# Optimization experiments

Hardware: AMD Instinct MI355X
Metric: run time of the kernel (lower is better)

Reference implementation:

```python
import jax, jax.numpy as jnp
import numpy as np

N_NODES = 100000
N_EDGES = 1600000
F_IN = 128
HIDDEN = 128
N_CLASSES = 2
N_GRAPHS = 512


def setup_inputs() -> dict:
    key = jax.random.key(0)
    ks = jax.random.split(key, 10)
    node_features = jax.random.normal(ks[0], (N_NODES, F_IN), dtype=jnp.float32)
    edge_index = jax.random.randint(ks[1], (2, N_EDGES), 0, N_NODES, dtype=jnp.int64)
    batch = jnp.sort(jax.random.randint(ks[2], (N_NODES,), 0, N_GRAPHS, dtype=jnp.int64))
    s1 = 1.0 / np.sqrt(F_IN)
    s2 = 1.0 / np.sqrt(HIDDEN)
    W1 = jax.random.uniform(ks[3], (F_IN, HIDDEN), jnp.float32, -s1, s1)
    b1 = jnp.zeros((HIDDEN,), jnp.float32)
    W2 = jax.random.uniform(ks[4], (HIDDEN, HIDDEN), jnp.float32, -s2, s2)
    b2 = jnp.zeros((HIDDEN,), jnp.float32)
    Wlin = jax.random.uniform(ks[5], (HIDDEN, N_CLASSES), jnp.float32, -s2, s2)
    blin = jax.random.uniform(ks[6], (N_CLASSES,), jnp.float32, -s2, s2)
    return {"node_features": node_features, "edge_index": edge_index, "batch": batch,
            "W1": W1, "b1": b1, "W2": W2, "b2": b2, "Wlin": Wlin, "blin": blin}


def _gcn_conv(x, src, dst, norm, W, b, n_nodes):
    # transform-then-propagate (PyG GCNConv default)
    h = x @ W                                   # [N, H]
    msg = h[src] * norm[:, None]                # gather + edge scale
    out = jax.ops.segment_sum(msg, dst, num_segments=n_nodes)  # scatter-add
    return out + b


def reference(node_features, edge_index, batch, W1, b1, W2, b2, Wlin, blin):
    n = node_features.shape[0]
    loop = jnp.arange(n, dtype=edge_index.dtype)
    src = jnp.concatenate([edge_index[0], loop])  # add self-loops
    dst = jnp.concatenate([edge_index[1], loop])
    # symmetric degree normalization: deg counts incoming edges incl. self-loop
    deg = jax.ops.segment_sum(jnp.ones_like(src, dtype=node_features.dtype), dst, num_segments=n)
    dis = jnp.where(deg > 0, jax.lax.rsqrt(jnp.maximum(deg, 1.0)), 0.0)
    norm = dis[src] * dis[dst]

    x = jax.nn.relu(_gcn_conv(node_features, src, dst, norm, W1, b1, n))
    x = jax.nn.relu(_gcn_conv(x, src, dst, norm, W2, b2, n))

    # global mean pool over graphs
    ones = jnp.ones((n,), dtype=x.dtype)
    counts = jax.ops.segment_sum(ones, batch, num_segments=N_GRAPHS)
    sums = jax.ops.segment_sum(x, batch, num_segments=N_GRAPHS)
    pooled = sums / jnp.maximum(counts, 1.0)[:, None]

    # dropout is identity in eval mode
    return pooled @ Wlin + blin
```

## Files before the change

### kernel.cpp

```cpp
#include <hip/hip_runtime.h>
#include <hip/hip_bf16.h>
#include <hip/hip_fp16.h>

constexpr int NN = 100000;
constexpr int NE = 1600000;
constexpr int NG = 512;
constexpr int F  = 128;

constexpr int NB   = 392;
constexpr int RCAP = 4608;
constexpr int CAP  = 32;
constexpr int NCH  = 8;
constexpr int BINB = 512;
constexpr int GEMB = (NN + 127) / 128;

typedef _Float16 f16;
typedef f16 f16x2 __attribute__((ext_vector_type(2)));
typedef f16 f16x4 __attribute__((ext_vector_type(4)));
typedef f16 f16x8 __attribute__((ext_vector_type(8)));
typedef float f32x4 __attribute__((ext_vector_type(4)));
typedef unsigned int u32;
typedef u32 u32x4a __attribute__((ext_vector_type(4), aligned(4)));

template<bool IN_HALF>
__device__ __forceinline__ void gemm_body(int bid, int tid,
                                          const void* __restrict__ Xv,
                                          const f16* __restrict__ WT,
                                          const float* __restrict__ dis,
                                          f16* __restrict__ H, int M) {
    const int wid = tid >> 6;
    const int lane = tid & 63;
    const int row0 = bid * 128;
    const int wrow = wid * 32;
    const int lr = lane & 15;
    const int lk = (lane >> 4) * 8;
    f32x4 acc[2][8] = {};
    #pragma unroll
    for (int ks = 0; ks < 4; ks++) {
        f16x8 a[2], b[8];
        #pragma unroll
        for (int mf = 0; mf < 2; mf++) {
            int row = row0 + wrow + mf * 16 + lr;
            row = row < M ? row : M - 1;
            if (IN_HALF) {
                a[mf] = *(const f16x8*)((const f16*)Xv + (size_t)row * 128 + ks * 32 + lk);
            } else {
                const float* Xf = (const float*)Xv + (size_t)row * 128 + ks * 32 + lk;
                float4 v0 = *(const float4*)Xf;
                float4 v1 = *(const float4*)(Xf + 4);
                a[mf] = f16x8{(f16)v0.x, (f16)v0.y, (f16)v0.z, (f16)v0.w,
                              (f16)v1.x, (f16)v1.y, (f16)v1.z, (f16)v1.w};
            }
        }
        #pragma unroll
        for (int nf = 0; nf < 8; nf++)
            b[nf] = *(const f16x8*)(WT + (size_t)(nf * 16 + lr) * 128 + ks * 32 + lk);
        #pragma unroll
        for (int mf = 0; mf < 2; mf++)
            #pragma unroll
            for (int nf = 0; nf < 8; nf++)
                acc[mf][nf] = __builtin_amdgcn_mfma_f32_16x16x32_f16(a[mf], b[nf], acc[mf][nf], 0, 0, 0);
    }
    const int crow = (lane >> 4) * 4;
    #pragma unroll
    for (int mf = 0; mf < 2; mf++) {
        #pragma unroll
        for (int reg = 0; reg < 4; reg++) {
            int row = row0 + wrow + mf * 16 + crow + reg;
            if (row < M) {
                float sc = dis[row];
                #pragma unroll
                for (int nf = 0; nf < 8; nf++)
                    H[(size_t)row * 128 + nf * 16 + lr] = (f16)(acc[mf][nf][reg] * sc);
            }
        }
    }
}

__global__ __launch_bounds__(256) void k1_bin_prepw(const int* __restrict__ ei,
                                                    int* __restrict__ gcur,
                                                    u32* __restrict__ binned,
                                                    const float* __restrict__ W1,
                                                    const float* __restrict__ W2,
                                                    f16* __restrict__ WT1,
                                                    f16* __restrict__ WT2) {
    __shared__ u32 stage[NB][CAP];
    __shared__ int scnt[NB];
    if (blockIdx.x >= BINB) {
        int idx = (blockIdx.x - BINB) * 256 + threadIdx.x;
        int n = idx >> 7, k = idx & 127;
        WT1[idx] = (f16)W1[k * 128 + n];
        WT2[idx] = (f16)W2[k * 128 + n];
        return;
    }
    for (int b = threadIdx.x; b < NB; b += 256) scnt[b] = 0;
    __syncthreads();
    const int per = NE / BINB;
    const int e0 = blockIdx.x * per;
    for (int r = 0; r < per; r += 256) {
        int k = r + threadIdx.x;
        if (k < per) {
            int e = e0 + k;
            int s = __builtin_nontemporal_load(&ei[e]);
            int d = __builtin_nontemporal_load(&ei[NE + e]);
            int b = d >> 8;
            u32 v = ((u32)(d & 255) << 24) | (u32)s;
            int p = atomicAdd(&scnt[b], 1);
            if (p < CAP) stage[b][p] = v;
        }
        __syncthreads();
        for (int b2 = threadIdx.x; b2 < NB; b2 += 256) {
            int n = scnt[b2];
            if (n >= 16) {
                int f = n & ~15;
                int base = b2 * RCAP + atomicAdd(&gcur[b2], f);
                const u32x4a* st4 = (const u32x4a*)&stage[b2][0];
                u32x4a* out4 = (u32x4a*)&binned[base];
                for (int j = 0; j < (f >> 2); j++) out4[j] = st4[j];
                for (int j = 0; j < n - f; j++) stage[b2][j] = stage[b2][f + j];
                scnt[b2] = n - f;
            }
        }
        __syncthreads();
    }
    for (int b2 = threadIdx.x; b2 < NB; b2 += 256) {
        int n = scnt[b2];
        if (n > 0) {
            int base = b2 * RCAP + atomicAdd(&gcur[b2], n);
            for (int j = 0; j < n; j++) binned[base + j] = stage[b2][j];
        }
    }
}

__global__ void scan_buckets(const int* __restrict__ gcur, int* __restrict__ bucketBase,
                             int* __restrict__ offs) {
    __shared__ int tmp[512];
    int t = threadIdx.x;
    int c = (t < NB) ? gcur[t] : 0;
    tmp[t] = c;
    __syncthreads();
    for (int d = 1; d < 512; d <<= 1) {
        int x = (t >= d) ? tmp[t - d] : 0;
        __syncthreads();
        tmp[t] += x;
        __syncthreads();
    }
    if (t < NB) bucketBase[t] = tmp[t] - c;
    if (t == 0) offs[NN] = NE;
}

__global__ __launch_bounds__(256) void k3_csr_gemm1(const u32* __restrict__ binned,
                                                    const int* __restrict__ gcur,
                                                    const int* __restrict__ bucketBase,
                                                    int* __restrict__ offs,
                                                    float* __restrict__ dis,
                                                    int* __restrict__ csr_src,
                                                    const float* __restrict__ X,
                                                    const f16* __restrict__ WT1,
                                                    const float* __restrict__ degdis,
                                                    f16* __restrict__ H) {
    __shared__ u32 ed[RCAP];
    __shared__ u32 lcsr[RCAP];
    __shared__ int hist[256];
    __shared__ int loff[256];
    __shared__ int lcur[256];
    if (blockIdx.x >= NB) {
        gemm_body<false>(blockIdx.x - NB, threadIdx.x, X, WT1, degdis, H, NN);
        return;
    }
    const int b = blockIdx.x;
    int cnt = gcur[b];
    if (cnt > RCAP) cnt = RCAP;
    const int gbase = bucketBase[b];
    const int t = threadIdx.x;
    hist[t] = 0;
    __syncthreads();
    for (int j = t; j < cnt; j += 256) {
        u32 v = __builtin_nontemporal_load(&binned[(size_t)b * RCAP + j]);
        ed[j] = v;
        atomicAdd(&hist[v >> 24], 1);
    }
    __syncthreads();
    int h = hist[t];
    loff[t] = h;
    __syncthreads();
    for (int d = 1; d < 256; d <<= 1) {
        int x = (t >= d) ? loff[t - d] : 0;
        __syncthreads();
        loff[t] += x;
        __syncthreads();
    }
    int excl = loff[t] - h;
    lcur[t] = excl;
    int node = (b << 8) + t;
    if (node < NN) {
        offs[node] = gbase + excl;
        dis[node] = rsqrtf((float)(h + 1));
    }
    __syncthreads();
    for (int j = t; j < cnt; j += 256) {
        u32 v = ed[j];
        int p = atomicAdd(&lcur[v >> 24], 1);
        lcsr[p] = v & 0x1FFFFu;
    }
    __syncthreads();
    for (int j = t; j < cnt; j += 256) csr_src[gbase + j] = (int)lcsr[j];
}


__device__ __forceinline__ void gather_rows_scaled(const f16* __restrict__ h, int i,
                                                   const int* __restrict__ offs,
                                                   const int* __restrict__ csr_src,
                                                   const float* __restrict__ dis,
                                                   int q, int r, float acc[8]) {
    if (q == 0) {
        f16x8 v = *(const f16x8*)(h + (size_t)i * F + r * 8);
        float di = dis[i];
        #pragma unroll
        for (int j = 0; j < 8; j++) acc[j] = (float)v[j] * di;
    }
    const int s = offs[i], e = offs[i + 1];
    int t = s + q;
    for (; t + 4 < e; t += 8) {
        int sr0 = csr_src[t];
        int sr1 = csr_src[t + 4];
        float d0 = dis[sr0], d1 = dis[sr1];
        f16x8 v0 = *(const f16x8*)(h + (size_t)sr0 * F + r * 8);
        f16x8 v1 = *(const f16x8*)(h + (size_t)sr1 * F + r * 8);
        #pragma unroll
        for (int j = 0; j < 8; j++)
            acc[j] += (float)v0[j] * d0 + (float)v1[j] * d1;
    }
    if (t < e) {
        int sr = csr_src[t];
        float d0 = dis[sr];
        f16x8 v = *(const f16x8*)(h + (size_t)sr * F + r * 8);
        #pragma unroll
        for (int j = 0; j < 8; j++) acc[j] += (float)v[j] * d0;
    }
    #pragma unroll
    for (int j = 0; j < 8; j++) {
        acc[j] += __shfl_xor(acc[j], 16);
        acc[j] += __shfl_xor(acc[j], 32);
    }
}

__device__ __forceinline__ void gather_rows(const f16* __restrict__ h, int i,
                                            const int* __restrict__ offs,
                                            const int* __restrict__ csr_src,
                                            int q, int r, float acc[8]) {
    if (q == 0) {
        f16x8 v = *(const f16x8*)(h + (size_t)i * F + r * 8);
        #pragma unroll
        for (int j = 0; j < 8; j++) acc[j] = (float)v[j];
    }
    const int s = offs[i], e = offs[i + 1];
    int t = s + q;
    for (; t + 4 < e; t += 8) {
        int sr0 = csr_src[t];
        int sr1 = csr_src[t + 4];
        f16x8 v0 = *(const f16x8*)(h + (size_t)sr0 * F + r * 8);
        f16x8 v1 = *(const f16x8*)(h + (size_t)sr1 * F + r * 8);
        #pragma unroll
        for (int j = 0; j < 8; j++) acc[j] += (float)v0[j] + (float)v1[j];
    }
    if (t < e) {
        int sr = csr_src[t];
        f16x8 v = *(const f16x8*)(h + (size_t)sr * F + r * 8);
        #pragma unroll
        for (int j = 0; j < 8; j++) acc[j] += (float)v[j];
    }
    #pragma unroll
    for (int j = 0; j < 8; j++) {
        acc[j] += __shfl_xor(acc[j], 16);
        acc[j] += __shfl_xor(acc[j], 32);
    }
}

__global__ __launch_bounds__(256) void aggregate_l1(const f16* __restrict__ h,
                                                    const int* __restrict__ offs,
                                                    const int* __restrict__ csr_src,
                                                    const float* __restrict__ dis,
                                                    const float* __restrict__ bias,
                                                    f16* __restrict__ out, int n) {
    int i = blockIdx.x * 4 + (threadIdx.x >> 6);
    if (i >= n) return;
    const int lane = threadIdx.x & 63;
    const int q = lane >> 4;
    const int r = lane & 15;
    float acc[8] = {};
    gather_rows_scaled(h, i, offs, csr_src, dis, q, r, acc);
    if (q == 0) {
        float di = dis[i];
        const float4* b4 = (const float4*)bias;
        float4 bb0 = b4[r * 2], bb1 = b4[r * 2 + 1];
        float bb[8] = {bb0.x, bb0.y, bb0.z, bb0.w, bb1.x, bb1.y, bb1.z, bb1.w};
        f16x8 o;
        #pragma unroll
        for (int j = 0; j < 8; j++) {
            float v = fmaf(acc[j], di, bb[j]);
            o[j] = (f16)(v > 0.f ? v : 0.f);
        }
        *(f16x8*)(out + (size_t)i * F + r * 8) = o;
    }
}

__global__ __launch_bounds__(256) void aggregate_l2(const f16* __restrict__ h,
                                                    const int* __restrict__ offs,
                                                    const int* __restrict__ csr_src,
                                                    const float* __restrict__ dis,
                                                    const float* __restrict__ bias,
                                                    f16* __restrict__ out, int n) {
    int i = blockIdx.x * 4 + (threadIdx.x >> 6);
    if (i >= n) return;
    const int lane = threadIdx.x & 63;
    const int q = lane >> 4;
    const int r = lane & 15;
    float acc[8] = {};
    gather_rows(h, i, offs, csr_src, q, r, acc);
    if (q == 0) {
        float di = dis[i];
        const float4* b4 = (const float4*)bias;
        float4 bb0 = b4[r * 2], bb1 = b4[r * 2 + 1];
        float bb[8] = {bb0.x, bb0.y, bb0.z, bb0.w, bb1.x, bb1.y, bb1.z, bb1.w};
        f16x8 o;
        #pragma unroll
        for (int j = 0; j < 8; j++) {
            float v = fmaf(acc[j], di, bb[j]);
            o[j] = (f16)(v > 0.f ? v : 0.f);
        }
        *(f16x8*)(out + (size_t)i * F + r * 8) = o;
    }
}

__global__ __launch_bounds__(256) void gemm2(const f16* __restrict__ Xh,
                                             const f16* __restrict__ WT,
                                             const float* __restrict__ dis,
                                             f16* __restrict__ H, int M) {
    gemm_body<true>(blockIdx.x, threadIdx.x, Xh, WT, dis, H, M);
}

__global__ __launch_bounds__(256) void pool_partial(const f16* __restrict__ x,
                                                    const int* __restrict__ batch,
                                                    float* __restrict__ partial, int n) {
    int g = blockIdx.x;
    __shared__ int se[2];
    if (threadIdx.x < 2) {
        int target = g + threadIdx.x;
        int lo = 0, hi = n;
        while (lo < hi) {
            int mid = (lo + hi) >> 1;
            if (batch[mid] < target) lo = mid + 1; else hi = mid;
        }
        se[threadIdx.x] = lo;
    }
    __syncthreads();
    int s = se[0], e = se[1];
    int wid = threadIdx.x >> 6, lane = threadIdx.x & 63;
    int slot = blockIdx.y * 4 + wid;
    float a0 = 0.f, a1 = 0.f;
    const f16x2* x2 = (const f16x2*)x;
    for (int i = s + slot; i < e; i += 4 * NCH) {
        f16x2 v = x2[(size_t)i * 64 + lane];
        a0 += (float)v[0];
        a1 += (float)v[1];
    }
    __shared__ float red[4][128];
    red[wid][lane * 2] = a0;
    red[wid][lane * 2 + 1] = a1;
    __syncthreads();
    if (wid == 0) {
        float s0 = red[0][lane * 2] + red[1][lane * 2] + red[2][lane * 2] + red[3][lane * 2];
        float s1 = red[0][lane * 2 + 1] + red[1][lane * 2 + 1] + red[2][lane * 2 + 1] + red[3][lane * 2 + 1];
        float2* pp = (float2*)&partial[((size_t)g * NCH + blockIdx.y) * F];
        pp[lane] = make_float2(s0, s1);
    }
}

__global__ __launch_bounds__(128) void pool_final(const float* __restrict__ partial,
                                                  const int* __restrict__ batch,
                                                  const float* __restrict__ Wlin,
                                                  const float* __restrict__ blin,
                                                  float* __restrict__ out, int n) {
    int g = blockIdx.x;
    int f = threadIdx.x;
    __shared__ int se[2];
    if (threadIdx.x < 2) {
        int target = g + threadIdx.x;
        int lo = 0, hi = n;
        while (lo < hi) {
            int mid = (lo + hi) >> 1;
            if (batch[mid] < target) lo = mid + 1; else hi = mid;
        }
        se[threadIdx.x] = lo;
    }
    __syncthreads();
    int s = se[0], e = se[1];
    float acc = 0.f;
    #pragma unroll
    for (int c = 0; c < NCH; c++) acc += partial[((size_t)g * NCH + c) * F + f];
    float cnt = (float)((e - s) > 0 ? (e - s) : 1);
    float p = acc / cnt;
    float v0 = p * Wlin[f * 2 + 0];
    float v1 = p * Wlin[f * 2 + 1];
    #pragma unroll
    for (int o = 32; o > 0; o >>= 1) {
        v0 += __shfl_xor(v0, o);
        v1 += __shfl_xor(v1, o);
    }
    __shared__ float red[4];
    int wid = threadIdx.x >> 6;
    if ((threadIdx.x & 63) == 0) { red[wid * 2] = v0; red[wid * 2 + 1] = v1; }
    __syncthreads();
    if (threadIdx.x == 0) {
        out[g * 2 + 0] = red[0] + red[2] + blin[0];
        out[g * 2 + 1] = red[1] + red[3] + blin[1];
    }
}

extern "C" void kernel_launch(void* const* d_in, const int* in_sizes, int n_in,
                              void* d_out, int out_size, void* d_ws, size_t ws_size,
                              hipStream_t stream) {
    const float* X     = (const float*)d_in[0];
    const int*   ei    = (const int*)d_in[1];
    const int*   batch = (const int*)d_in[2];
    const float* W1    = (const float*)d_in[3];
    const float* b1    = (const float*)d_in[4];
    const float* W2    = (const float*)d_in[5];
    const float* b2    = (const float*)d_in[6];
    const float* Wlin  = (const float*)d_in[7];
    const float* blin  = (const float*)d_in[8];
    float* out = (float*)d_out;

    char* p = (char*)d_ws;
    auto alloc = [&](size_t bytes) -> char* {
        char* r = p;
        p += (bytes + 255) & ~size_t(255);
        return r;
    };
    int*   gcur       = (int*)alloc((size_t)NB * 4);
    int*   bucketBase = (int*)alloc((size_t)NB * 4);
    int*   offs       = (int*)alloc((size_t)(NN + 1) * 4);
    float* dis        = (float*)alloc((size_t)NN * 4);
    u32*   binned     = (u32*)alloc((size_t)NB * RCAP * 4);
    int*   csr_src    = (int*)alloc((size_t)NE * 4);
    f16*   WT1        = (f16*)alloc((size_t)128 * 128 * 2);
    f16*   WT2        = (f16*)alloc((size_t)128 * 128 * 2);
    f16*   bufA       = (f16*)alloc((size_t)NN * F * 2);
    f16*   bufB       = (f16*)alloc((size_t)NN * F * 2);
    float* partial    = (float*)alloc((size_t)NG * NCH * F * 4);
    float* ones       = (float*)alloc((size_t)NN * 4);

    hipMemsetAsync(gcur, 0, (size_t)NB * 4, stream);
    extern __global__ void fill_ones(float*, int);
    fill_ones<<<(NN + 255) / 256, 256, 0, stream>>>(ones, NN);

    k1_bin_prepw<<<BINB + 64, 256, 0, stream>>>(ei, gcur, binned, W1, W2, WT1, WT2);
    scan_buckets<<<1, 512, 0, stream>>>(gcur, bucketBase, offs);
    k3_csr_gemm1<<<NB + GEMB, 256, 0, stream>>>(binned, gcur, bucketBase, offs, dis,
                                                csr_src, X, WT1, ones, bufA);

    aggregate_l1<<<(NN + 3) / 4, 256, 0, stream>>>(bufA, offs, csr_src, dis, b1, bufB, NN);
    gemm2<<<GEMB, 256, 0, stream>>>(bufB, WT2, dis, bufA, NN);
    aggregate_l2<<<(NN + 3) / 4, 256, 0, stream>>>(bufA, offs, csr_src, dis, b2, bufB, NN);
    pool_partial<<<dim3(NG, NCH), 256, 0, stream>>>(bufB, batch, partial, NN);
    pool_final<<<NG, 128, 0, stream>>>(partial, batch, Wlin, blin, out, NN);
}

__global__ void fill_ones(float* __restrict__ v, int n) {
    int i = blockIdx.x * blockDim.x + threadIdx.x;
    if (i < n) v[i] = 1.0f;
}
```

Measured before the change: 262.7 us.

## Fuse layer-1 aggregation with GEMM2 and layer-2 aggregation with pooling

Layer-1 aggregation now writes each wave's 32 output rows into shared memory, and GEMM2 runs on them in the same kernel. This removes a full N×128 fp16 round-trip and one launch. Layer-2 aggregation accumulates per-graph sums in registers and flushes them with atomics into a single partial buffer, which replaces the separate pool_partial kernel and its second buffer read. The fill_ones kernel is dropped by templating away the scale in GEMM1. The cost is much fewer aggregation waves in flight (each wave walks 32 rows serially instead of one), which may hurt latency hiding for the random gathers, plus float atomic contention and non-deterministic summation order.

```diff
diff --git a/kernel.cpp b/kernel.cpp
--- a/kernel.cpp
+++ b/kernel.cpp
@@ -10,9 +10,9 @@
 constexpr int NB   = 392;
 constexpr int RCAP = 4608;
 constexpr int CAP  = 32;
-constexpr int NCH  = 8;
 constexpr int BINB = 512;
 constexpr int GEMB = (NN + 127) / 128;
+constexpr int F2B  = (NN + 63) / 64;
 
 typedef _Float16 f16;
 typedef f16 f16x2 __attribute__((ext_vector_type(2)));
@@ -21,61 +21,6 @@
 typedef float f32x4 __attribute__((ext_vector_type(4)));
 typedef unsigned int u32;
 typedef u32 u32x4a __attribute__((ext_vector_type(4), aligned(4)));
-
-template<bool IN_HALF>
-__device__ __forceinline__ void gemm_body(int bid, int tid,
-                                          const void* __restrict__ Xv,
-                                          const f16* __restrict__ WT,
-                                          const float* __restrict__ dis,
-                                          f16* __restrict__ H, int M) {
-    const int wid = tid >> 6;
-    const int lane = tid & 63;
-    const int row0 = bid * 128;
-    const int wrow = wid * 32;
-    const int lr = lane & 15;
-    const int lk = (lane >> 4) * 8;
-    f32x4 acc[2][8] = {};
-    #pragma unroll
-    for (int ks = 0; ks < 4; ks++) {
-        f16x8 a[2], b[8];
-        #pragma unroll
-        for (int mf = 0; mf < 2; mf++) {
-            int row = row0 + wrow + mf * 16 + lr;
-            row = row < M ? row : M - 1;
-            if (IN_HALF) {
-                a[mf] = *(const f16x8*)((const f16*)Xv + (size_t)row * 128 + ks * 32 + lk);
-            } else {
-                const float* Xf = (const float*)Xv + (size_t)row * 128 + ks * 32 + lk;
-                float4 v0 = *(const float4*)Xf;
-                float4 v1 = *(const float4*)(Xf + 4);
-                a[mf] = f16x8{(f16)v0.x, (f16)v0.y, (f16)v0.z, (f16)v0.w,
-                              (f16)v1.x, (f16)v1.y, (f16)v1.z, (f16)v1.w};
-            }
-        }
-        #pragma unroll
-        for (int nf = 0; nf < 8; nf++)
-            b[nf] = *(const f16x8*)(WT + (size_t)(nf * 16 + lr) * 128 + ks * 32 + lk);
-        #pragma unroll
-        for (int mf = 0; mf < 2; mf++)
-            #pragma unroll
-            for (int nf = 0; nf < 8; nf++)
-                acc[mf][nf] = __builtin_amdgcn_mfma_f32_16x16x32_f16(a[mf], b[nf], acc[mf][nf], 0, 0, 0);
-    }
-    const int crow = (lane >> 4) * 4;
-    #pragma unroll
-    for (int mf = 0; mf < 2; mf++) {
-        #pragma unroll
-        for (int reg = 0; reg < 4; reg++) {
-            int row = row0 + wrow + mf * 16 + crow + reg;
-            if (row < M) {
-                float sc = dis[row];
-                #pragma unroll
-                for (int nf = 0; nf < 8; nf++)
-                    H[(size_t)row * 128 + nf * 16 + lr] = (f16)(acc[mf][nf][reg] * sc);
-            }
-        }
-    }
-}
 
 __global__ __launch_bounds__(256) void k1_bin_prepw(const int* __restrict__ ei,
                                                     int* __restrict__ gcur,
@@ -149,6 +94,61 @@
     if (t == 0) offs[NN] = NE;
 }
 
+template<bool IN_HALF, bool SCALE>
+__device__ __forceinline__ void gemm_body(int bid, int tid,
+                                          const void* __restrict__ Xv,
+                                          const f16* __restrict__ WT,
+                                          const float* __restrict__ dis,
+                                          f16* __restrict__ H, int M) {
+    const int wid = tid >> 6;
+    const int lane = tid & 63;
+    const int row0 = bid * 128;
+    const int wrow = wid * 32;
+    const int lr = lane & 15;
+    const int lk = (lane >> 4) * 8;
+    f32x4 acc[2][8] = {};
+    #pragma unroll
+    for (int ks = 0; ks < 4; ks++) {
+        f16x8 a[2], b[8];
+        #pragma unroll
+        for (int mf = 0; mf < 2; mf++) {
+            int row = row0 + wrow + mf * 16 + lr;
+            row = row < M ? row : M - 1;
+            if (IN_HALF) {
+                a[mf] = *(const f16x8*)((const f16*)Xv + (size_t)row * 128 + ks * 32 + lk);
+            } else {
+                const float* Xf = (const float*)Xv + (size_t)row * 128 + ks * 32 + lk;
+                float4 v0 = *(const float4*)Xf;
+                float4 v1 = *(const float4*)(Xf + 4);
+                a[mf] = f16x8{(f16)v0.x, (f16)v0.y, (f16)v0.z, (f16)v0.w,
+                              (f16)v1.x, (f16)v1.y, (f16)v1.z, (f16)v1.w};
+            }
+        }
+        #pragma unroll
+        for (int nf = 0; nf < 8; nf++)
+            b[nf] = *(const f16x8*)(WT + (size_t)(nf * 16 + lr) * 128 + ks * 32 + lk);
+        #pragma unroll
+        for (int mf = 0; mf < 2; mf++)
+            #pragma unroll
+            for (int nf = 0; nf < 8; nf++)
+                acc[mf][nf] = __builtin_amdgcn_mfma_f32_16x16x32_f16(a[mf], b[nf], acc[mf][nf], 0, 0, 0);
+    }
+    const int crow = (lane >> 4) * 4;
+    #pragma unroll
+    for (int mf = 0; mf < 2; mf++) {
+        #pragma unroll
+        for (int reg = 0; reg < 4; reg++) {
+            int row = row0 + wrow + mf * 16 + crow + reg;
+            if (row < M) {
+                float sc = SCALE ? dis[row] : 1.0f;
+                #pragma unroll
+                for (int nf = 0; nf < 8; nf++)
+                    H[(size_t)row * 128 + nf * 16 + lr] = (f16)(acc[mf][nf][reg] * sc);
+            }
+        }
+    }
+}
+
 __global__ __launch_bounds__(256) void k3_csr_gemm1(const u32* __restrict__ binned,
                                                     const int* __restrict__ gcur,
                                                     const int* __restrict__ bucketBase,
@@ -157,7 +157,6 @@
                                                     int* __restrict__ csr_src,
                                                     const float* __restrict__ X,
                                                     const f16* __restrict__ WT1,
-                                                    const float* __restrict__ degdis,
                                                     f16* __restrict__ H) {
     __shared__ u32 ed[RCAP];
     __shared__ u32 lcsr[RCAP];
@@ -165,7 +164,7 @@
     __shared__ int loff[256];
     __shared__ int lcur[256];
     if (blockIdx.x >= NB) {
-        gemm_body<false>(blockIdx.x - NB, threadIdx.x, X, WT1, degdis, H, NN);
+        gemm_body<false, false>(blockIdx.x - NB, threadIdx.x, X, WT1, nullptr, H, NN);
         return;
     }
     const int b = blockIdx.x;
@@ -206,7 +205,6 @@
     __syncthreads();
     for (int j = t; j < cnt; j += 256) csr_src[gbase + j] = (int)lcsr[j];
 }
-
 
 __device__ __forceinline__ void gather_rows_scaled(const f16* __restrict__ h, int i,
                                                    const int* __restrict__ offs,
@@ -277,103 +275,116 @@
     }
 }
 
-__global__ __launch_bounds__(256) void aggregate_l1(const f16* __restrict__ h,
-                                                    const int* __restrict__ offs,
-                                                    const int* __restrict__ csr_src,
-                                                    const float* __restrict__ dis,
-                                                    const float* __restrict__ bias,
-                                                    f16* __restrict__ out, int n) {
-    int i = blockIdx.x * 4 + (threadIdx.x >> 6);
-    if (i >= n) return;
+__global__ __launch_bounds__(256) void fused_agg1_gemm2(const f16* __restrict__ h1,
+                                                        const int* __restrict__ offs,
+                                                        const int* __restrict__ csr_src,
+                                                        const float* __restrict__ dis,
+                                                        const float* __restrict__ bias,
+                                                        const f16* __restrict__ WT2,
+                                                        f16* __restrict__ H, int n) {
+    __shared__ f16 sX[4][32 * 136];
+    const int wid = threadIdx.x >> 6;
     const int lane = threadIdx.x & 63;
     const int q = lane >> 4;
     const int r = lane & 15;
-    float acc[8] = {};
-    gather_rows_scaled(h, i, offs, csr_src, dis, q, r, acc);
-    if (q == 0) {
-        float di = dis[i];
-        const float4* b4 = (const float4*)bias;
-        float4 bb0 = b4[r * 2], bb1 = b4[r * 2 + 1];
-        float bb[8] = {bb0.x, bb0.y, bb0.z, bb0.w, bb1.x, bb1.y, bb1.z, bb1.w};
-        f16x8 o;
-        #pragma unroll
-        for (int j = 0; j < 8; j++) {
-            float v = fmaf(acc[j], di, bb[j]);
-            o[j] = (f16)(v > 0.f ? v : 0.f);
-        }
-        *(f16x8*)(out + (size_t)i * F + r * 8) = o;
-    }
-}
-
-__global__ __launch_bounds__(256) void aggregate_l2(const f16* __restrict__ h,
-                                                    const int* __restrict__ offs,
-                                                    const int* __restrict__ csr_src,
-                                                    const float* __restrict__ dis,
-                                                    const float* __restrict__ bias,
-                                                    f16* __restrict__ out, int n) {
-    int i = blockIdx.x * 4 + (threadIdx.x >> 6);
-    if (i >= n) return;
+    const int row0 = blockIdx.x * 128 + wid * 32;
+    const float4* b4 = (const float4*)bias;
+    float4 bb0 = b4[r * 2], bb1 = b4[r * 2 + 1];
+    float bb[8] = {bb0.x, bb0.y, bb0.z, bb0.w, bb1.x, bb1.y, bb1.z, bb1.w};
+    for (int m = 0; m < 32; m++) {
+        int i = row0 + m;
+        i = i < n ? i : n - 1;
+        float acc[8] = {};
+        gather_rows_scaled(h1, i, offs, csr_src, dis, q, r, acc);
+        if (q == 0) {
+            float di = dis[i];
+            f16x8 o;
+            #pragma unroll
+            for (int j = 0; j < 8; j++) {
+                float v = fmaf(acc[j], di, bb[j]);
+                o[j] = (f16)(v > 0.f ? v : 0.f);
+            }
+            *(f16x8*)&sX[wid][m * 136 + r * 8] = o;
+        }
+    }
+    const int lk = (lane >> 4) * 8;
+    f32x4 acc2[2][8] = {};
+    #pragma unroll
+    for (int ks = 0; ks < 4; ks++) {
+        f16x8 a[2], b[8];
+        #pragma unroll
+        for (int mf = 0; mf < 2; mf++)
+            a[mf] = *(const f16x8*)&sX[wid][(mf * 16 + r) * 136 + ks * 32 + lk];
+        #pragma unroll
+        for (int nf = 0; nf < 8; nf++)
+            b[nf] = *(const f16x8*)(WT2 + (size_t)(nf * 16 + r) * 128 + ks * 32 + lk);
+        #pragma unroll
+        for (int mf = 0; mf < 2; mf++)
+            #pragma unroll
+            for (int nf = 0; nf < 8; nf++)
+                acc2[mf][nf] = __builtin_amdgcn_mfma_f32_16x16x32_f16(a[mf], b[nf], acc2[mf][nf], 0, 0, 0);
+    }
+    const int crow = (lane >> 4) * 4;
+    #pragma unroll
+    for (int mf = 0; mf < 2; mf++) {
+        #pragma unroll
+        for (int reg = 0; reg < 4; reg++) {
+            int row = row0 + mf * 16 + crow + reg;
+            if (row < n) {
+                float sc = dis[row];
+                #pragma unroll
+                for (int nf = 0; nf < 8; nf++)
+                    H[(size_t)row * 128 + nf * 16 + r] = (f16)(acc2[mf][nf][reg] * sc);
+            }
+        }
+    }
+}
+
+__global__ __launch_bounds__(256) void fused_agg2_pool(const f16* __restrict__ h2,
+                                                       const int* __restrict__ offs,
+                                                       const int* __restrict__ csr_src,
+                                                       const float* __restrict__ dis,
+                                                       const float* __restrict__ bias,
+                                                       const int* __restrict__ batch,
+                                                       float* __restrict__ partial, int n) {
+    const int wid = threadIdx.x >> 6;
     const int lane = threadIdx.x & 63;
     const int q = lane >> 4;
     const int r = lane & 15;
-    float acc[8] = {};
-    gather_rows(h, i, offs, csr_src, q, r, acc);
-    if (q == 0) {
+    const int base = blockIdx.x * 64 + wid * 16;
+    if (base >= n) return;
+    const float4* b4 = (const float4*)bias;
+    float4 bb0 = b4[r * 2], bb1 = b4[r * 2 + 1];
+    float bb[8] = {bb0.x, bb0.y, bb0.z, bb0.w, bb1.x, bb1.y, bb1.z, bb1.w};
+    float pacc[8] = {};
+    int cur_g = -1;
+    for (int m = 0; m < 16; m++) {
+        int i = base + m;
+        if (i >= n) break;
+        float acc[8] = {};
+        gather_rows(h2, i, offs, csr_src, q, r, acc);
+        int g = batch[i];
+        if (g != cur_g) {
+            if (cur_g >= 0 && q == 0) {
+                #pragma unroll
+                for (int j = 0; j < 8; j++)
+                    atomicAdd(&partial[(size_t)cur_g * F + r * 8 + j], pacc[j]);
+            }
+            #pragma unroll
+            for (int j = 0; j < 8; j++) pacc[j] = 0.f;
+            cur_g = g;
+        }
         float di = dis[i];
-        const float4* b4 = (const float4*)bias;
-        float4 bb0 = b4[r * 2], bb1 = b4[r * 2 + 1];
-        float bb[8] = {bb0.x, bb0.y, bb0.z, bb0.w, bb1.x, bb1.y, bb1.z, bb1.w};
-        f16x8 o;
         #pragma unroll
         for (int j = 0; j < 8; j++) {
             float v = fmaf(acc[j], di, bb[j]);
-            o[j] = (f16)(v > 0.f ? v : 0.f);
-        }
-        *(f16x8*)(out + (size_t)i * F + r * 8) = o;
-    }
-}
-
-__global__ __launch_bounds__(256) void gemm2(const f16* __restrict__ Xh,
-                                             const f16* __restrict__ WT,
-                                             const float* __restrict__ dis,
-                                             f16* __restrict__ H, int M) {
-    gemm_body<true>(blockIdx.x, threadIdx.x, Xh, WT, dis, H, M);
-}
-
-__global__ __launch_bounds__(256) void pool_partial(const f16* __restrict__ x,
-                                                    const int* __restrict__ batch,
-                                                    float* __restrict__ partial, int n) {
-    int g = blockIdx.x;
-    __shared__ int se[2];
-    if (threadIdx.x < 2) {
-        int target = g + threadIdx.x;
-        int lo = 0, hi = n;
-        while (lo < hi) {
-            int mid = (lo + hi) >> 1;
-            if (batch[mid] < target) lo = mid + 1; else hi = mid;
-        }
-        se[threadIdx.x] = lo;
-    }
-    __syncthreads();
-    int s = se[0], e = se[1];
-    int wid = threadIdx.x >> 6, lane = threadIdx.x & 63;
-    int slot = blockIdx.y * 4 + wid;
-    float a0 = 0.f, a1 = 0.f;
-    const f16x2* x2 = (const f16x2*)x;
-    for (int i = s + slot; i < e; i += 4 * NCH) {
-        f16x2 v = x2[(size_t)i * 64 + lane];
-        a0 += (float)v[0];
-        a1 += (float)v[1];
-    }
-    __shared__ float red[4][128];
-    red[wid][lane * 2] = a0;
-    red[wid][lane * 2 + 1] = a1;
-    __syncthreads();
-    if (wid == 0) {
-        float s0 = red[0][lane * 2] + red[1][lane * 2] + red[2][lane * 2] + red[3][lane * 2];
-        float s1 = red[0][lane * 2 + 1] + red[1][lane * 2 + 1] + red[2][lane * 2 + 1] + red[3][lane * 2 + 1];
-        float2* pp = (float2*)&partial[((size_t)g * NCH + blockIdx.y) * F];
-        pp[lane] = make_float2(s0, s1);
+            pacc[j] += v > 0.f ? v : 0.f;
+        }
+    }
+    if (cur_g >= 0 && q == 0) {
+        #pragma unroll
+        for (int j = 0; j < 8; j++)
+            atomicAdd(&partial[(size_t)cur_g * F + r * 8 + j], pacc[j]);
     }
 }
 
@@ -396,11 +407,8 @@
     }
     __syncthreads();
     int s = se[0], e = se[1];
-    float acc = 0.f;
-    #pragma unroll
-    for (int c = 0; c < NCH; c++) acc += partial[((size_t)g * NCH + c) * F + f];
     float cnt = (float)((e - s) > 0 ? (e - s) : 1);
-    float p = acc / cnt;
+    float p = partial[(size_t)g * F + f] / cnt;
     float v0 = p * Wlin[f * 2 + 0];
     float v1 = p * Wlin[f * 2 + 1];
     #pragma unroll
@@ -447,27 +455,17 @@
     f16*   WT1        = (f16*)alloc((size_t)128 * 128 * 2);
     f16*   WT2        = (f16*)alloc((size_t)128 * 128 * 2);
     f16*   bufA       = (f16*)alloc((size_t)NN * F * 2);
-    f16*   bufB       = (f16*)alloc((size_t)NN * F * 2);
-    float* partial    = (float*)alloc((size_t)NG * NCH * F * 4);
-    float* ones       = (float*)alloc((size_t)NN * 4);
+    f16*   bufC       = (f16*)alloc((size_t)NN * F * 2);
+    float* partial    = (float*)alloc((size_t)NG * F * 4);
 
     hipMemsetAsync(gcur, 0, (size_t)NB * 4, stream);
-    extern __global__ void fill_ones(float*, int);
-    fill_ones<<<(NN + 255) / 256, 256, 0, stream>>>(ones, NN);
+    hipMemsetAsync(partial, 0, (size_t)NG * F * 4, stream);
 
     k1_bin_prepw<<<BINB + 64, 256, 0, stream>>>(ei, gcur, binned, W1, W2, WT1, WT2);
     scan_buckets<<<1, 512, 0, stream>>>(gcur, bucketBase, offs);
     k3_csr_gemm1<<<NB + GEMB, 256, 0, stream>>>(binned, gcur, bucketBase, offs, dis,
-                                                csr_src, X, WT1, ones, bufA);
-
-    aggregate_l1<<<(NN + 3) / 4, 256, 0, stream>>>(bufA, offs, csr_src, dis, b1, bufB, NN);
-    gemm2<<<GEMB, 256, 0, stream>>>(bufB, WT2, dis, bufA, NN);
-    aggregate_l2<<<(NN + 3) / 4, 256, 0, stream>>>(bufA, offs, csr_src, dis, b2, bufB, NN);
-    pool_partial<<<dim3(NG, NCH), 256, 0, stream>>>(bufB, batch, partial, NN);
+                                                csr_src, X, WT1, bufA);
+    fused_agg1_gemm2<<<GEMB, 256, 0, stream>>>(bufA, offs, csr_src, dis, b1, WT2, bufC, NN);
+    fused_agg2_pool<<<F2B, 256, 0, stream>>>(bufC, offs, csr_src, dis, b2, batch, partial, NN);
     pool_final<<<NG, 128, 0, stream>>>(partial, batch, Wlin, blin, out, NN);
 }
-
-__global__ void fill_ones(float* __restrict__ v, int n) {
-    int i = blockIdx.x * blockDim.x + threadIdx.x;
-    if (i < n) v[i] = 1.0f;
-}
```

Measured after the change: 370.1 us. +40.8%, slower.
